# Kernel tuning notes

Measured on AMD Instinct MI355X. Metric: run time of the kernel, lower is better.

## Reference

```python
import jax, jax.numpy as jnp
import numpy as np

B, S, D = 4, 4096, 1024

def setup_inputs() -> dict:
    key = jax.random.key(0)
    ks = jax.random.split(key, 11)
    scale = 1.0 / np.sqrt(D)
    def lin(k):
        return jax.random.normal(k, (D, D), dtype=jnp.float32) * scale
    return {
        "x": jax.random.normal(ks[0], (B, S, D), dtype=jnp.float32),
        "Wq": lin(ks[1]), "bq": jax.random.normal(ks[2], (D,), dtype=jnp.float32) * 0.02,
        "Wk": lin(ks[3]), "bk": jax.random.normal(ks[4], (D,), dtype=jnp.float32) * 0.02,
        "Wv": lin(ks[5]), "bv": jax.random.normal(ks[6], (D,), dtype=jnp.float32) * 0.02,
        "W1": lin(ks[7]), "b1": jax.random.normal(ks[8], (D,), dtype=jnp.float32) * 0.02,
        "W2": lin(ks[9]), "b2": jax.random.normal(ks[10], (D,), dtype=jnp.float32) * 0.02,
    }

def reference(x, Wq, bq, Wk, bk, Wv, bv, W1, b1, W2, b2):
    d = x.shape[-1]
    # Single-head self-attention with residual (faithful to source)
    q = x @ Wq + bq  # [B,S,D]
    k = x @ Wk + bk
    v = x @ Wv + bv
    scores = jnp.einsum('bsd,btd->bst', q, k) / jnp.sqrt(jnp.float32(d))  # [B,S,S]
    attn = jax.nn.softmax(scores, axis=-1)
    x = x + jnp.einsum('bst,btd->bsd', attn, v)
    # FeedForward: fc2(relu(fc1(x))), then doubled (x = x + x in source)
    h = jax.nn.relu(x @ W1 + b1)
    y = h @ W2 + b2
    return y + y
```

## Files before the change

kernel.cpp:

```cpp
#include <hip/hip_runtime.h>
#include <stdint.h>

typedef unsigned short u16;
typedef __bf16 bf16x8 __attribute__((ext_vector_type(8)));
typedef float f32x4 __attribute__((ext_vector_type(4)));
typedef unsigned short u16x8 __attribute__((ext_vector_type(8)));
typedef unsigned short u16x4 __attribute__((ext_vector_type(4)));

__device__ __forceinline__ float b2f(u16 b) {
    return __uint_as_float(((unsigned)b) << 16);
}
__device__ __forceinline__ u16 f2b(float f) {
    unsigned u = __float_as_uint(f);
    unsigned r = (u + 0x7fffu + ((u >> 16) & 1u)) >> 16;
    return (u16)r;
}

#define GLDS16(g, l) __builtin_amdgcn_global_load_lds(                        \
    (const __attribute__((address_space(1))) void*)(g),                       \
    (__attribute__((address_space(3))) void*)(l), 16, 0, 0)

#define BAR()  __builtin_amdgcn_s_barrier()
#define LG0()  do { asm volatile("s_waitcnt lgkmcnt(0)" ::: "memory");        \
                    __builtin_amdgcn_sched_barrier(0); } while (0)
#define WVM4() asm volatile("s_waitcnt vmcnt(4)" ::: "memory")
#define WVM0() asm volatile("s_waitcnt vmcnt(0)" ::: "memory")

template<int HAS_BIAS, int RELU, int HAS_RES, int OUT_MODE>
__device__ __forceinline__ void gemm13_body(
    const u16* __restrict__ A, const u16* __restrict__ Bt,
    const float* __restrict__ bias, const float* __restrict__ res,
    void* __restrict__ Cout, int N, int K,
    long sA, long sB, long sC, long sR, float scale)
{
    __shared__ u16 smem[65536];

    const long nwg = (long)gridDim.x * gridDim.y * gridDim.z;
    long gid = ((long)blockIdx.z * gridDim.y + blockIdx.y) * gridDim.x + blockIdx.x;
    long logical = (nwg % 8 == 0) ? (gid & 7) * (nwg >> 3) + (gid >> 3) : gid;
    const int bx = (int)(logical % gridDim.x);
    long tmp = logical / gridDim.x;
    const int by = (int)(tmp % gridDim.y);
    const int bz = (int)(tmp / gridDim.y);

    A  += (long)bz * sA;
    Bt += (long)bz * sB;

    const int tid  = threadIdx.x;
    const int lane = tid & 63, wid = tid >> 6;
    const int wm   = wid >> 2, wn = wid & 3;
    const int lr   = lane & 15, lk = lane >> 4;
    const long m0  = (long)by * 256;
    const long n0  = (long)bx * 256;
    const int  NT  = K >> 6;

    const int sch = ((tid & 3) ^ ((tid >> 3) & 3)) * 8;
    const u16* gA0 = A  + (m0 + (tid >> 2)) * (long)K + sch;
    const u16* gB0 = Bt + (n0 + (tid >> 2)) * (long)K + sch;
    const u16* gA1 = gA0 + 128L * K;
    const u16* gB1 = gB0 + 128L * K;
    const int wdst = (tid & ~63) * 8;

#define STA(bufn, kh, kof) do {                                               \
    GLDS16(gA0 + (kof) + (kh) * 32, &smem[(bufn)*16384 + (kh)*8192 + wdst]);  \
    GLDS16(gA1 + (kof) + (kh) * 32, &smem[(bufn)*16384 + (kh)*8192 + wdst + 4096]); } while (0)
#define STB(bufn, kh, kof) do {                                               \
    GLDS16(gB0 + (kof) + (kh) * 32, &smem[32768 + (bufn)*16384 + (kh)*8192 + wdst]); \
    GLDS16(gB1 + (kof) + (kh) * 32, &smem[32768 + (bufn)*16384 + (kh)*8192 + wdst + 4096]); } while (0)

    const int lkA    = lk ^ ((lr >> 1) & 3);
    const int raBase = (wm * 128 + lr) * 32 + lkA * 8;
    const int rbBase = (wn * 64  + lr) * 32 + lkA * 8;

#define LDA(c, kh) do { _Pragma("unroll")                                     \
    for (int i = 0; i < 8; ++i)                                               \
        a[i] = *(const bf16x8*)&smem[(c)*16384 + (kh)*8192 + raBase + i*512]; } while (0)
#define LDB(c, kh, nh) do { _Pragma("unroll")                                 \
    for (int jj = 0; jj < 2; ++jj)                                            \
        b[jj] = *(const bf16x8*)&smem[32768 + (c)*16384 + (kh)*8192 + rbBase + (nh)*1024 + jj*512]; } while (0)

#define MFMA_Q(nh) do { __builtin_amdgcn_s_setprio(1); _Pragma("unroll")      \
    for (int i = 0; i < 8; ++i) _Pragma("unroll")                             \
        for (int jj = 0; jj < 2; ++jj)                                        \
            acc[i][(nh)*2 + jj] = __builtin_amdgcn_mfma_f32_16x16x32_bf16(    \
                a[i], b[jj], acc[i][(nh)*2 + jj], 0, 0, 0);                   \
    __builtin_amdgcn_s_setprio(0); } while (0)

    f32x4 acc[8][4];
    #pragma unroll
    for (int i = 0; i < 8; ++i)
        #pragma unroll
        for (int j = 0; j < 4; ++j)
            #pragma unroll
            for (int r = 0; r < 4; ++r) acc[i][j][r] = 0.0f;

    STA(0, 0, 0); STB(0, 0, 0); STA(0, 1, 0); STB(0, 1, 0);
    WVM4();
    BAR();

    #pragma unroll 1
    for (int t = 0; t < NT; ++t) {
        const int cur = t & 1, nxt = cur ^ 1;
        const long kN = (long)(t + 1) * 64;
        const bool st = (t + 1 < NT);
        bf16x8 a[8], b[2];

        LDA(cur, 0); LDB(cur, 0, 0);
        if (st) STA(nxt, 0, kN);
        BAR(); LG0();
        MFMA_Q(0);
        BAR();
        LDB(cur, 0, 1);
        if (st) STB(nxt, 0, kN);
        BAR(); LG0();
        MFMA_Q(1);
        if (st) { WVM4(); } else { WVM0(); }
        BAR();
        LDA(cur, 1); LDB(cur, 1, 1);
        if (st) STA(nxt, 1, kN);
        BAR(); LG0();
        MFMA_Q(1);
        BAR();
        LDB(cur, 1, 0);
        if (st) STB(nxt, 1, kN);
        BAR(); LG0();
        MFMA_Q(0);
        if (st) { WVM4(); } else { WVM0(); }
        BAR();
    }

    const long crow0 = m0 + wm * 128;
    const long ccol0 = n0 + wn * 64;
    u16*   Cb = (u16*)Cout   + (long)bz * sC;
    float* Cf = (float*)Cout + (long)bz * sC;
    const float* resz = res + (long)bz * sR;
    #pragma unroll
    for (int i = 0; i < 8; ++i) {
        #pragma unroll
        for (int j = 0; j < 4; ++j) {
            const long col = ccol0 + j * 16 + lr;
            float bv_ = 0.0f;
            if (HAS_BIAS) bv_ = bias[col];
            if (OUT_MODE == 2) {
                const long row0 = crow0 + i * 16 + lk * 4;
                u16x4 pk;
                #pragma unroll
                for (int r = 0; r < 4; ++r) {
                    float v = acc[i][j][r] + bv_;
                    v *= scale;
                    pk[r] = f2b(v);
                }
                const long b_ = row0 >> 12, s_ = row0 & 4095;
                *(u16x4*)((u16*)Cout + (b_ << 22) + (col << 12) + s_) = pk;
            } else {
                #pragma unroll
                for (int r = 0; r < 4; ++r) {
                    const long row = crow0 + i * 16 + lk * 4 + r;
                    float v = acc[i][j][r];
                    if (HAS_BIAS) v += bv_;
                    v *= scale;
                    if (RELU) v = fmaxf(v, 0.0f);
                    if (HAS_RES) v += resz[row * (long)N + col];
                    if (OUT_MODE == 1) Cf[row * (long)N + col] = v;
                    else               Cb[row * (long)N + col] = f2b(v);
                }
            }
        }
    }
#undef STA
#undef STB
#undef LDA
#undef LDB
#undef MFMA_Q
}

__global__ __launch_bounds__(512, 2) void g13_proj(
    const u16* A, const u16* Bt, const float* bias, u16* C, int N, int K)
{ gemm13_body<1,0,0,0>(A, Bt, bias, nullptr, C, N, K, 0,0,0,0, 1.0f); }

__global__ __launch_bounds__(512, 2) void g13_vproj(
    const u16* A, const u16* Bt, const float* bias, u16* C, int N, int K)
{ gemm13_body<1,0,0,2>(A, Bt, bias, nullptr, C, N, K, 0,0,0,0, 1.0f); }

__global__ __launch_bounds__(512, 2) void g13_qkt(
    const u16* A, const u16* Bt, u16* C, int N, int K,
    long sA, long sB, long sC, float scale)
{ gemm13_body<0,0,0,0>(A, Bt, nullptr, nullptr, C, N, K, sA, sB, sC, 0, scale); }

__global__ __launch_bounds__(512, 2) void g13_pv(
    const u16* A, const u16* Bt, const float* res, u16* C, int N, int K,
    long sA, long sB, long sC, long sR)
{ gemm13_body<0,0,1,0>(A, Bt, nullptr, res, C, N, K, sA, sB, sC, sR, 1.0f); }

__global__ __launch_bounds__(512, 2) void g13_ffn1(
    const u16* A, const u16* Bt, const float* bias, u16* C, int N, int K)
{ gemm13_body<1,1,0,0>(A, Bt, bias, nullptr, C, N, K, 0,0,0,0, 1.0f); }

__global__ __launch_bounds__(512, 2) void g13_ffn2(
    const u16* A, const u16* Bt, const float* bias, float* C, int N, int K, float scale)
{ gemm13_body<1,0,0,1>(A, Bt, bias, nullptr, C, N, K, 0,0,0,0, scale); }

__global__ __launch_bounds__(256) void cvt_f32_bf16(
    const float* __restrict__ in, u16* __restrict__ out, long n)
{
    long i = ((long)blockIdx.x * 256 + threadIdx.x) * 4;
    if (i >= n) return;
    float4 f = *(const float4*)(in + i);
    u16x4 o;
    o[0] = f2b(f.x); o[1] = f2b(f.y); o[2] = f2b(f.z); o[3] = f2b(f.w);
    *(u16x4*)(out + i) = o;
}

__global__ __launch_bounds__(256) void transpose_to_bf16(
    const float* __restrict__ in, u16* __restrict__ out, int R, int C)
{
    __shared__ float tile[32][33];
    const int bx = blockIdx.x * 32;
    const int by = blockIdx.y * 32;
    const int tx = threadIdx.x, ty = threadIdx.y;
    #pragma unroll
    for (int i = 0; i < 32; i += 8)
        tile[ty + i][tx] = in[(long)(by + ty + i) * C + bx + tx];
    __syncthreads();
    #pragma unroll
    for (int i = 0; i < 32; i += 8)
        out[(long)(bx + ty + i) * R + by + tx] = f2b(tile[tx][ty + i]);
}

__global__ __launch_bounds__(256) void softmax_rows(u16* __restrict__ P, int n)
{
    const int t = threadIdx.x;
    const int lane = t & 63, w = t >> 6;
    u16* row = P + (long)blockIdx.x * n;
    u16x8 a = *(const u16x8*)(row + t * 16);
    u16x8 b = *(const u16x8*)(row + t * 16 + 8);
    float v[16];
    #pragma unroll
    for (int i = 0; i < 8; ++i) { v[i] = b2f(a[i]); v[8 + i] = b2f(b[i]); }

    float mx = v[0];
    #pragma unroll
    for (int i = 1; i < 16; ++i) mx = fmaxf(mx, v[i]);
    #pragma unroll
    for (int o = 32; o > 0; o >>= 1) mx = fmaxf(mx, __shfl_xor(mx, o));
    __shared__ float red[8];
    if (lane == 0) red[w] = mx;
    __syncthreads();
    mx = fmaxf(fmaxf(red[0], red[1]), fmaxf(red[2], red[3]));

    float s = 0.0f;
    #pragma unroll
    for (int i = 0; i < 16; ++i) { v[i] = __expf(v[i] - mx); s += v[i]; }
    #pragma unroll
    for (int o = 32; o > 0; o >>= 1) s += __shfl_xor(s, o);
    if (lane == 0) red[4 + w] = s;
    __syncthreads();
    s = red[4] + red[5] + red[6] + red[7];
    const float inv = 1.0f / s;

    #pragma unroll
    for (int i = 0; i < 8; ++i) { a[i] = f2b(v[i] * inv); b[i] = f2b(v[8 + i] * inv); }
    *(u16x8*)(row + t * 16)     = a;
    *(u16x8*)(row + t * 16 + 8) = b;
}

extern "C" void kernel_launch(void* const* d_in, const int* in_sizes, int n_in,
                              void* d_out, int out_size, void* d_ws, size_t ws_size,
                              hipStream_t stream)
{
    (void)in_sizes; (void)n_in; (void)out_size;
    const float* x  = (const float*)d_in[0];
    const float* Wq = (const float*)d_in[1];
    const float* bq = (const float*)d_in[2];
    const float* Wk = (const float*)d_in[3];
    const float* bk = (const float*)d_in[4];
    const float* Wv = (const float*)d_in[5];
    const float* bv = (const float*)d_in[6];
    const float* W1 = (const float*)d_in[7];
    const float* b1 = (const float*)d_in[8];
    const float* W2 = (const float*)d_in[9];
    const float* b2 = (const float*)d_in[10];
    float* out = (float*)d_out;

    const int  B = 4, S = 4096, D = 1024;
    const long SD  = (long)S * D;
    const long BSD = (long)B * SD;
    const long SS  = (long)S * S;

    int BC = 4;
    while (BC > 1 && (size_t)((long)BC * SS + 5L * D * D + 3L * BSD) * 2 > ws_size)
        BC >>= 1;

    u16* Pb = (u16*)d_ws;
    u16* xb = Pb;
    u16* Wt = Pb + (long)BC * SS;
    u16* Qb = Wt + 5L * D * D;
    u16* Kb = Qb + BSD;
    u16* Vt = Kb + BSD;

    cvt_f32_bf16<<<dim3((unsigned)(BSD / 4 / 256)), 256, 0, stream>>>(x, xb, BSD);

    dim3 tb(32, 8);
    transpose_to_bf16<<<dim3(D / 32, D / 32), tb, 0, stream>>>(Wq, Wt + 0L * D * D, D, D);
    transpose_to_bf16<<<dim3(D / 32, D / 32), tb, 0, stream>>>(Wk, Wt + 1L * D * D, D, D);
    transpose_to_bf16<<<dim3(D / 32, D / 32), tb, 0, stream>>>(Wv, Wt + 2L * D * D, D, D);
    transpose_to_bf16<<<dim3(D / 32, D / 32), tb, 0, stream>>>(W1, Wt + 3L * D * D, D, D);
    transpose_to_bf16<<<dim3(D / 32, D / 32), tb, 0, stream>>>(W2, Wt + 4L * D * D, D, D);

    const dim3 gproj(D / 256, (B * S) / 256);
    g13_proj <<<gproj, 512, 0, stream>>>(xb, Wt + 0L*D*D, bq, Qb, D, D);
    g13_proj <<<gproj, 512, 0, stream>>>(xb, Wt + 1L*D*D, bk, Kb, D, D);
    g13_vproj<<<gproj, 512, 0, stream>>>(xb, Wt + 2L*D*D, bv, Vt, D, D);

    for (int c = 0; c < B; c += BC) {
        g13_qkt<<<dim3(S/256, S/256, BC), 512, 0, stream>>>(
            Qb + (long)c * SD, Kb + (long)c * SD, Pb, S, D, SD, SD, SS, 0.03125f);
        softmax_rows<<<BC * S, 256, 0, stream>>>(Pb, S);
        g13_pv<<<dim3(D/256, S/256, BC), 512, 0, stream>>>(
            Pb, Vt + (long)c * SD, x + (long)c * SD, Kb + (long)c * SD,
            D, S, SS, SD, SD, SD);
    }

    g13_ffn1<<<gproj, 512, 0, stream>>>(Kb, Wt + 3L*D*D, b1, Qb, D, D);
    g13_ffn2<<<gproj, 512, 0, stream>>>(Qb, Wt + 4L*D*D, b2, out, D, D, 2.0f);
}
```

Before: 530.5 us.

## Add software-pipelined GEMM variant for QK^T and batch weight transposes into one launch

Introduces a new GEMM body that interleaves LDS fragment reads, async global-to-LDS loads of the next K tile, and MFMA blocks in a finer-grained schedule with explicit lgkmcnt/vmcnt waits and setprio around the MFMAs. Only the QK^T score kernel uses it; the other GEMMs keep the previous body. The five weight-transpose launches are merged into a single 3D-grid launch to cut launch overhead. The hand-scheduled wait counts are fragile and could stall or mis-order loads if the counts are off.

```diff
diff --git a/kernel.cpp b/kernel.cpp
--- a/kernel.cpp
+++ b/kernel.cpp
@@ -25,6 +25,166 @@
                     __builtin_amdgcn_sched_barrier(0); } while (0)
 #define WVM4() asm volatile("s_waitcnt vmcnt(4)" ::: "memory")
 #define WVM0() asm volatile("s_waitcnt vmcnt(0)" ::: "memory")
+
+template<int HAS_BIAS, int RELU, int HAS_RES, int OUT_MODE>
+__device__ __forceinline__ void gemm11_body(
+    const u16* __restrict__ A, const u16* __restrict__ Bt,
+    const float* __restrict__ bias, const float* __restrict__ res,
+    void* __restrict__ Cout, int N, int K,
+    long sA, long sB, long sC, long sR, float scale)
+{
+    __shared__ u16 smem[65536];
+
+    const long nwg = (long)gridDim.x * gridDim.y * gridDim.z;
+    long gid = ((long)blockIdx.z * gridDim.y + blockIdx.y) * gridDim.x + blockIdx.x;
+    long logical = (nwg % 8 == 0) ? (gid & 7) * (nwg >> 3) + (gid >> 3) : gid;
+    const int bx = (int)(logical % gridDim.x);
+    long tmp = logical / gridDim.x;
+    const int by = (int)(tmp % gridDim.y);
+    const int bz = (int)(tmp / gridDim.y);
+
+    A  += (long)bz * sA;
+    Bt += (long)bz * sB;
+
+    const int tid  = threadIdx.x;
+    const int lane = tid & 63, wid = tid >> 6;
+    const int wm   = wid >> 2, wn = wid & 3;
+    const int lr   = lane & 15, lk = lane >> 4;
+    const long m0  = (long)by * 256;
+    const long n0  = (long)bx * 256;
+    const int  NT  = K >> 6;
+
+    const int sch = ((tid & 3) ^ ((tid >> 3) & 3)) * 8;
+    const u16* gA0 = A  + (m0 + (tid >> 2)) * (long)K + sch;
+    const u16* gB0 = Bt + (n0 + (tid >> 2)) * (long)K + sch;
+    const u16* gA1 = gA0 + 128L * K;
+    const u16* gB1 = gB0 + 128L * K;
+    const int wdst = (tid & ~63) * 8;
+
+#define STA(bufn, kk, kof) do {                                               \
+    GLDS16(gA0 + (kof) + (kk) * 32, &smem[(bufn)*16384 + (kk)*8192 + wdst]);  \
+    GLDS16(gA1 + (kof) + (kk) * 32, &smem[(bufn)*16384 + (kk)*8192 + wdst + 4096]); } while (0)
+#define STB(bufn, kk, kof) do {                                               \
+    GLDS16(gB0 + (kof) + (kk) * 32, &smem[32768 + (bufn)*16384 + (kk)*8192 + wdst]); \
+    GLDS16(gB1 + (kof) + (kk) * 32, &smem[32768 + (bufn)*16384 + (kk)*8192 + wdst + 4096]); } while (0)
+
+    const int lkA   = lk ^ ((lr >> 1) & 3);
+    const int raOff = (wm * 128 + lr) * 32 + lkA * 8;
+    const int rbOff = (wn * 64  + lr) * 32 + lkA * 8;
+
+#define DSA(dst, BUF, kk, ih) do { _Pragma("unroll")                          \
+    for (int i = 0; i < 4; ++i)                                               \
+        dst[i] = *(const bf16x8*)&smem[(BUF)*16384 + (kk)*8192 + raOff + ((ih)*4 + i)*512]; } while (0)
+#define DSB(dst, BUF, kk) do { _Pragma("unroll")                              \
+    for (int j = 0; j < 4; ++j)                                               \
+        dst[j] = *(const bf16x8*)&smem[32768 + (BUF)*16384 + (kk)*8192 + rbOff + j*512]; } while (0)
+
+#define LGK(n) do { asm volatile("s_waitcnt lgkmcnt(" #n ")" ::: "memory");   \
+                    __builtin_amdgcn_sched_barrier(0); } while (0)
+#define CKPT(n) do { asm volatile("s_waitcnt vmcnt(" #n ")" ::: "memory");    \
+    __builtin_amdgcn_s_barrier(); __builtin_amdgcn_sched_barrier(0); } while (0)
+
+#define MFM(IH, A_, B_) do { __builtin_amdgcn_s_setprio(1); _Pragma("unroll") \
+    for (int i = 0; i < 4; ++i) _Pragma("unroll")                             \
+        for (int j = 0; j < 4; ++j)                                           \
+            acc[(IH)*4 + i][j] = __builtin_amdgcn_mfma_f32_16x16x32_bf16(     \
+                A_[i], B_[j], acc[(IH)*4 + i][j], 0, 0, 0);                   \
+    __builtin_amdgcn_s_setprio(0); } while (0)
+
+#define TILE_MAIN(BUF, kof) do {                                              \
+    DSA(aY, BUF, 0, 1);                 STA((BUF)^1, 0, kof);                 \
+    LGK(4);  MFM(0, aX, bX);                                                  \
+    CKPT(2);                                                                  \
+    DSA(aX, BUF, 1, 0);  DSB(bY, BUF, 1);  STB((BUF)^1, 0, kof);              \
+    LGK(8);  MFM(1, aY, bX);                                                  \
+    DSA(aY, BUF, 1, 1);                 STA((BUF)^1, 1, kof);                 \
+    LGK(4);  MFM(0, aX, bY);                                                  \
+    CKPT(2);                                                                  \
+    DSA(aX, (BUF)^1, 0, 0);  DSB(bX, (BUF)^1, 0);  STB((BUF)^1, 1, kof);      \
+    LGK(8);  MFM(1, aY, bY);                                                  \
+} while (0)
+
+#define TILE_LAST(BUF) do {                                                   \
+    DSA(aY, BUF, 0, 1);                                                       \
+    LGK(4);  MFM(0, aX, bX);                                                  \
+    CKPT(0);                                                                  \
+    DSA(aX, BUF, 1, 0);  DSB(bY, BUF, 1);                                     \
+    LGK(8);  MFM(1, aY, bX);                                                  \
+    DSA(aY, BUF, 1, 1);                                                       \
+    LGK(4);  MFM(0, aX, bY);                                                  \
+    LGK(0);  MFM(1, aY, bY);                                                  \
+} while (0)
+
+    f32x4 acc[8][4];
+    #pragma unroll
+    for (int i = 0; i < 8; ++i)
+        #pragma unroll
+        for (int j = 0; j < 4; ++j)
+            #pragma unroll
+            for (int r = 0; r < 4; ++r) acc[i][j][r] = 0.0f;
+
+    bf16x8 aX[4], aY[4], bX[4], bY[4];
+
+    STA(0, 0, 0); STB(0, 0, 0); STA(0, 1, 0); STB(0, 1, 0);
+    CKPT(4);
+    DSA(aX, 0, 0, 0); DSB(bX, 0, 0);
+
+    #pragma unroll 1
+    for (int t = 0; t + 2 < NT; t += 2) {
+        TILE_MAIN(0, (long)(t + 1) * 64);
+        TILE_MAIN(1, (long)(t + 2) * 64);
+    }
+    TILE_MAIN(0, (long)(NT - 1) * 64);
+    TILE_LAST(1);
+
+    const long crow0 = m0 + wm * 128;
+    const long ccol0 = n0 + wn * 64;
+    u16*   Cb = (u16*)Cout   + (long)bz * sC;
+    float* Cf = (float*)Cout + (long)bz * sC;
+    const float* resz = res + (long)bz * sR;
+    #pragma unroll
+    for (int i = 0; i < 8; ++i) {
+        #pragma unroll
+        for (int j = 0; j < 4; ++j) {
+            const long col = ccol0 + j * 16 + lr;
+            float bv_ = 0.0f;
+            if (HAS_BIAS) bv_ = bias[col];
+            if (OUT_MODE == 2) {
+                const long row0 = crow0 + i * 16 + lk * 4;
+                u16x4 pk;
+                #pragma unroll
+                for (int r = 0; r < 4; ++r) {
+                    float v = acc[i][j][r] + bv_;
+                    v *= scale;
+                    pk[r] = f2b(v);
+                }
+                const long b_ = row0 >> 12, s_ = row0 & 4095;
+                *(u16x4*)((u16*)Cout + (b_ << 22) + (col << 12) + s_) = pk;
+            } else {
+                #pragma unroll
+                for (int r = 0; r < 4; ++r) {
+                    const long row = crow0 + i * 16 + lk * 4 + r;
+                    float v = acc[i][j][r];
+                    if (HAS_BIAS) v += bv_;
+                    v *= scale;
+                    if (RELU) v = fmaxf(v, 0.0f);
+                    if (HAS_RES) v += resz[row * (long)N + col];
+                    if (OUT_MODE == 1) Cf[row * (long)N + col] = v;
+                    else               Cb[row * (long)N + col] = f2b(v);
+                }
+            }
+        }
+    }
+#undef STA
+#undef STB
+#undef DSA
+#undef DSB
+#undef LGK
+#undef CKPT
+#undef MFM
+#undef TILE_MAIN
+#undef TILE_LAST
+}
 
 template<int HAS_BIAS, int RELU, int HAS_RES, int OUT_MODE>
 __device__ __forceinline__ void gemm13_body(
@@ -174,29 +334,29 @@
 #undef MFMA_Q
 }
 
-__global__ __launch_bounds__(512, 2) void g13_proj(
+__global__ __launch_bounds__(512, 2) void g14_qkt(
+    const u16* A, const u16* Bt, u16* C, int N, int K,
+    long sA, long sB, long sC, float scale)
+{ gemm11_body<0,0,0,0>(A, Bt, nullptr, nullptr, C, N, K, sA, sB, sC, 0, scale); }
+
+__global__ __launch_bounds__(512, 2) void g14_proj(
     const u16* A, const u16* Bt, const float* bias, u16* C, int N, int K)
 { gemm13_body<1,0,0,0>(A, Bt, bias, nullptr, C, N, K, 0,0,0,0, 1.0f); }
 
-__global__ __launch_bounds__(512, 2) void g13_vproj(
+__global__ __launch_bounds__(512, 2) void g14_vproj(
     const u16* A, const u16* Bt, const float* bias, u16* C, int N, int K)
 { gemm13_body<1,0,0,2>(A, Bt, bias, nullptr, C, N, K, 0,0,0,0, 1.0f); }
 
-__global__ __launch_bounds__(512, 2) void g13_qkt(
-    const u16* A, const u16* Bt, u16* C, int N, int K,
-    long sA, long sB, long sC, float scale)
-{ gemm13_body<0,0,0,0>(A, Bt, nullptr, nullptr, C, N, K, sA, sB, sC, 0, scale); }
-
-__global__ __launch_bounds__(512, 2) void g13_pv(
+__global__ __launch_bounds__(512, 2) void g14_pv(
     const u16* A, const u16* Bt, const float* res, u16* C, int N, int K,
     long sA, long sB, long sC, long sR)
 { gemm13_body<0,0,1,0>(A, Bt, nullptr, res, C, N, K, sA, sB, sC, sR, 1.0f); }
 
-__global__ __launch_bounds__(512, 2) void g13_ffn1(
+__global__ __launch_bounds__(512, 2) void g14_ffn1(
     const u16* A, const u16* Bt, const float* bias, u16* C, int N, int K)
 { gemm13_body<1,1,0,0>(A, Bt, bias, nullptr, C, N, K, 0,0,0,0, 1.0f); }
 
-__global__ __launch_bounds__(512, 2) void g13_ffn2(
+__global__ __launch_bounds__(512, 2) void g14_ffn2(
     const u16* A, const u16* Bt, const float* bias, float* C, int N, int K, float scale)
 { gemm13_body<1,0,0,1>(A, Bt, bias, nullptr, C, N, K, 0,0,0,0, scale); }
 
@@ -211,20 +371,26 @@
     *(u16x4*)(out + i) = o;
 }
 
-__global__ __launch_bounds__(256) void transpose_to_bf16(
-    const float* __restrict__ in, u16* __restrict__ out, int R, int C)
-{
+__global__ __launch_bounds__(256) void transpose5_to_bf16(
+    const float* __restrict__ Wq, const float* __restrict__ Wk,
+    const float* __restrict__ Wv, const float* __restrict__ W1,
+    const float* __restrict__ W2, u16* __restrict__ out, int Dm)
+{
+    const int z = blockIdx.z;
+    const float* in = (z == 0) ? Wq : (z == 1) ? Wk : (z == 2) ? Wv
+                    : (z == 3) ? W1 : W2;
+    u16* o = out + (long)z * Dm * Dm;
     __shared__ float tile[32][33];
     const int bx = blockIdx.x * 32;
     const int by = blockIdx.y * 32;
     const int tx = threadIdx.x, ty = threadIdx.y;
     #pragma unroll
     for (int i = 0; i < 32; i += 8)
-        tile[ty + i][tx] = in[(long)(by + ty + i) * C + bx + tx];
+        tile[ty + i][tx] = in[(long)(by + ty + i) * Dm + bx + tx];
     __syncthreads();
     #pragma unroll
     for (int i = 0; i < 32; i += 8)
-        out[(long)(bx + ty + i) * R + by + tx] = f2b(tile[tx][ty + i]);
+        o[(long)(bx + ty + i) * Dm + by + tx] = f2b(tile[tx][ty + i]);
 }
 
 __global__ __launch_bounds__(256) void softmax_rows(u16* __restrict__ P, int n)
@@ -300,27 +466,23 @@
 
     cvt_f32_bf16<<<dim3((unsigned)(BSD / 4 / 256)), 256, 0, stream>>>(x, xb, BSD);
 
-    dim3 tb(32, 8);
-    transpose_to_bf16<<<dim3(D / 32, D / 32), tb, 0, stream>>>(Wq, Wt + 0L * D * D, D, D);
-    transpose_to_bf16<<<dim3(D / 32, D / 32), tb, 0, stream>>>(Wk, Wt + 1L * D * D, D, D);
-    transpose_to_bf16<<<dim3(D / 32, D / 32), tb, 0, stream>>>(Wv, Wt + 2L * D * D, D, D);
-    transpose_to_bf16<<<dim3(D / 32, D / 32), tb, 0, stream>>>(W1, Wt + 3L * D * D, D, D);
-    transpose_to_bf16<<<dim3(D / 32, D / 32), tb, 0, stream>>>(W2, Wt + 4L * D * D, D, D);
+    transpose5_to_bf16<<<dim3(D / 32, D / 32, 5), dim3(32, 8), 0, stream>>>(
+        Wq, Wk, Wv, W1, W2, Wt, D);
 
     const dim3 gproj(D / 256, (B * S) / 256);
-    g13_proj <<<gproj, 512, 0, stream>>>(xb, Wt + 0L*D*D, bq, Qb, D, D);
-    g13_proj <<<gproj, 512, 0, stream>>>(xb, Wt + 1L*D*D, bk, Kb, D, D);
-    g13_vproj<<<gproj, 512, 0, stream>>>(xb, Wt + 2L*D*D, bv, Vt, D, D);
+    g14_proj <<<gproj, 512, 0, stream>>>(xb, Wt + 0L*D*D, bq, Qb, D, D);
+    g14_proj <<<gproj, 512, 0, stream>>>(xb, Wt + 1L*D*D, bk, Kb, D, D);
+    g14_vproj<<<gproj, 512, 0, stream>>>(xb, Wt + 2L*D*D, bv, Vt, D, D);
 
     for (int c = 0; c < B; c += BC) {
-        g13_qkt<<<dim3(S/256, S/256, BC), 512, 0, stream>>>(
+        g14_qkt<<<dim3(S/256, S/256, BC), 512, 0, stream>>>(
             Qb + (long)c * SD, Kb + (long)c * SD, Pb, S, D, SD, SD, SS, 0.03125f);
         softmax_rows<<<BC * S, 256, 0, stream>>>(Pb, S);
-        g13_pv<<<dim3(D/256, S/256, BC), 512, 0, stream>>>(
+        g14_pv<<<dim3(D/256, S/256, BC), 512, 0, stream>>>(
             Pb, Vt + (long)c * SD, x + (long)c * SD, Kb + (long)c * SD,
             D, S, SS, SD, SD, SD);
     }
 
-    g13_ffn1<<<gproj, 512, 0, stream>>>(Kb, Wt + 3L*D*D, b1, Qb, D, D);
-    g13_ffn2<<<gproj, 512, 0, stream>>>(Qb, Wt + 4L*D*D, b2, out, D, D, 2.0f);
-}
+    g14_ffn1<<<gproj, 512, 0, stream>>>(Kb, Wt + 3L*D*D, b1, Qb, D, D);
+    g14_ffn2<<<gproj, 512, 0, stream>>>(Qb, Wt + 4L*D*D, b2, out, D, D, 2.0f);
+}
```

After: 534.6 us. Within noise of the previous version (+0.8%).
